# Performance work log

Hardware: AMD Instinct MI355X
Metric: run time of the kernel (lower is better)

## Reference

```python
import jax, jax.numpy as jnp
import numpy as np

D_MODEL = 1024
N_HEADS = 16


def setup_inputs() -> dict:
    key = jax.random.key(0)
    k1, k2, k3 = jax.random.split(key, 3)
    B, S = 2, 2048
    std_qkv = (2.0 / (D_MODEL + 3 * D_MODEL)) ** 0.5
    std_out = (2.0 / (D_MODEL + D_MODEL)) ** 0.5
    X = jax.random.normal(k1, (B, S, D_MODEL), dtype=jnp.float32)
    W_qkv = jax.random.normal(k2, (3 * D_MODEL, D_MODEL), dtype=jnp.float32) * std_qkv
    W_out = jax.random.normal(k3, (D_MODEL, D_MODEL), dtype=jnp.float32) * std_out
    return {"X": X, "W_qkv": W_qkv, "W_out": W_out}


def reference(X, W_qkv, W_out):
    B, S, D = X.shape
    H = N_HEADS
    dk = D // H
    # qkv projection: (..., d) @ W^T -> (..., 3d)
    qkv = jnp.einsum('bsd,ed->bse', X, W_qkv)
    Q, K, V = jnp.split(qkv, 3, axis=-1)
    # split heads: (B, S, H*dk) -> (B, H, S, dk)
    def heads(t):
        return t.reshape(B, S, H, dk).transpose(0, 2, 1, 3)
    Q, K, V = heads(Q), heads(K), heads(V)
    # scaled scores (B, H, S, S)
    scores = jnp.einsum('bhqd,bhkd->bhqk', Q, K) / jnp.sqrt(jnp.float32(dk))
    causal = jnp.tril(jnp.ones((S, S), dtype=bool))
    scores = jnp.where(causal, scores.astype(jnp.float32), -jnp.inf)
    weights = jax.nn.softmax(scores, axis=-1).astype(X.dtype)
    out = jnp.einsum('bhqk,bhkd->bhqd', weights, V)
    out = out.transpose(0, 2, 1, 3).reshape(B, S, D)
    return jnp.einsum('bsd,od->bso', out, W_out)
```

## Files before the change

### kernel.cpp

```cpp
#include <hip/hip_runtime.h>

typedef __bf16 bf16;
typedef __bf16 bf16x4v __attribute__((ext_vector_type(4)));
typedef __bf16 bf16x8 __attribute__((ext_vector_type(8)));
typedef float f32x4 __attribute__((ext_vector_type(4)));

#define MFMA16(a, b, c) __builtin_amdgcn_mfma_f32_16x16x32_bf16((a), (b), (c), 0, 0, 0)

#if __has_builtin(__builtin_amdgcn_exp2f)
#define EXP2(x) __builtin_amdgcn_exp2f(x)
#else
#define EXP2(x) exp2f(x)
#endif

#define SEQ 2048
#define DM 1024
#define NH 16

typedef __attribute__((address_space(3))) unsigned int lds_u32;
typedef __attribute__((address_space(1))) const unsigned int glb_u32;

__device__ __forceinline__ void gld16(const bf16* g, bf16* l) {
    __builtin_amdgcn_global_load_lds((glb_u32*)g, (lds_u32*)l, 16, 0, 0);
}

__global__ __launch_bounds__(256) void cvt_all(const float* __restrict__ X,
                                               const float* __restrict__ Wq,
                                               const float* __restrict__ Wo,
                                               bf16* __restrict__ Xb,
                                               bf16* __restrict__ Wqb,
                                               bf16* __restrict__ Wob) {
    const int i = blockIdx.x * 256 + threadIdx.x;
    const int N1 = (4 * 1024 * 1024) / 4;
    const int N2 = (3 * 1024 * 1024) / 4;
    const float* s; bf16* d; int off;
    if (i < N1)            { s = X;  d = Xb;  off = i; }
    else if (i < N1 + N2)  { s = Wq; d = Wqb; off = i - N1; }
    else                   { s = Wo; d = Wob; off = i - N1 - N2; }
    const float4 v = ((const float4*)s)[off];
    bf16x4v o;
    o.x = (bf16)v.x; o.y = (bf16)v.y; o.z = (bf16)v.z; o.w = (bf16)v.w;
    ((bf16x4v*)d)[off] = o;
}

__global__ __launch_bounds__(256) void gemm_qkv(const bf16* __restrict__ A,
                                                const bf16* __restrict__ B,
                                                bf16* __restrict__ qkbuf,
                                                bf16* __restrict__ vtg) {
    __shared__ bf16 smem[16384];
    bf16* As = smem;
    bf16* Bs = smem + 8192;

    const int K = DM, tid = threadIdx.x;
    const int lane = tid & 63, w = tid >> 6;
    const int quad = lane >> 4, l15 = lane & 15;
    const int wm = (w & 1) * 64, wn = (w >> 1) * 64;

    const int nbx = gridDim.x;
    const int orig = blockIdx.y * nbx + blockIdx.x;
    const int cpx = (nbx * gridDim.y) >> 3;
    const int swz = (orig & 7) * cpx + (orig >> 3);
    const int rowBase = (swz / nbx) * 128, colBase = (swz % nbx) * 128;
    const bool isV = (colBase >= 2 * DM);

    f32x4 acc[4][4] = {};

    auto stage = [&](int k0) {
#pragma unroll
        for (int i = 0; i < 4; ++i) {
            const int c = i * 256 + tid;
            const int row = c >> 3;
            const int sg = (c & 7) ^ (row & 7);
            gld16(A + (size_t)(rowBase + row) * K + k0 + sg * 8,
                  As + (i * 256 + w * 64) * 8);
            gld16(B + (size_t)(colBase + row) * K + k0 + sg * 8,
                  Bs + (i * 256 + w * 64) * 8);
        }
    };

    stage(0);

    for (int k0 = 0; k0 < K; k0 += 64) {
        __syncthreads();

        bf16x8 af[2][4], bfr[2][4];
#pragma unroll
        for (int ks = 0; ks < 2; ++ks)
#pragma unroll
            for (int i = 0; i < 4; ++i) {
                const int ra = wm + i * 16 + l15;
                af[ks][i]  = *(const bf16x8*)(As + ra * 64 + (((ks * 4 + quad) ^ (ra & 7)) * 8));
                const int rb = wn + i * 16 + l15;
                bfr[ks][i] = *(const bf16x8*)(Bs + rb * 64 + (((ks * 4 + quad) ^ (rb & 7)) * 8));
            }

        __syncthreads();

        if (k0 + 64 < K) stage(k0 + 64);

        if (isV) {
#pragma unroll
            for (int ks = 0; ks < 2; ++ks)
#pragma unroll
                for (int i = 0; i < 4; ++i)
#pragma unroll
                    for (int j = 0; j < 4; ++j)
                        acc[i][j] = MFMA16(af[ks][i], bfr[ks][j], acc[i][j]);
        } else {
#pragma unroll
            for (int ks = 0; ks < 2; ++ks)
#pragma unroll
                for (int i = 0; i < 4; ++i)
#pragma unroll
                    for (int j = 0; j < 4; ++j)
                        acc[i][j] = MFMA16(bfr[ks][j], af[ks][i], acc[i][j]);
        }
    }

    if (!isV) {
#pragma unroll
        for (int i = 0; i < 4; ++i)
#pragma unroll
            for (int j = 0; j < 4; ++j) {
                bf16x4v pk;
#pragma unroll
                for (int r = 0; r < 4; ++r) pk[r] = (bf16)acc[i][j][r];
                *(bf16x4v*)(qkbuf + (size_t)(rowBase + wm + i * 16 + l15) * 2048 +
                            colBase + wn + j * 16 + quad * 4) = pk;
            }
    } else {
        bf16* T = smem;
        const int vcolBase = colBase - 2 * DM;
        const int bb = rowBase >> 11;
        const int sBase = rowBase & 2047;
        const int drow0 = tid >> 4, seg = tid & 15;
#pragma unroll
        for (int c = 0; c < 2; ++c) {
            __syncthreads();
            if ((w >> 1) == c) {
#pragma unroll
                for (int i = 0; i < 4; ++i)
#pragma unroll
                    for (int j = 0; j < 4; ++j) {
                        bf16x4v pk;
#pragma unroll
                        for (int r = 0; r < 4; ++r) pk[r] = (bf16)acc[i][j][r];
                        *(bf16x4v*)(T + (j * 16 + l15) * 136 + wm + i * 16 + quad * 4) = pk;
                    }
            }
            __syncthreads();
#pragma unroll
            for (int rr = 0; rr < 4; ++rr) {
                const int drow = rr * 16 + drow0;
                *(bf16x8*)(vtg + (size_t)(bb * DM + vcolBase + c * 64 + drow) * SEQ +
                           sBase + seg * 8) =
                    *(const bf16x8*)(T + drow * 136 + seg * 8);
            }
        }
    }
}

__global__ __launch_bounds__(256) void gemm_out(const bf16* __restrict__ A,
                                                const bf16* __restrict__ B,
                                                float* __restrict__ C) {
    __shared__ bf16 As[64 * 64];
    __shared__ bf16 Bs[128 * 64];

    const int K = DM, N = DM, tid = threadIdx.x;
    const int lane = tid & 63, w = tid >> 6;
    const int quad = lane >> 4, l15 = lane & 15;
    const int wm = (w & 1) * 32, wn = (w >> 1) * 64;

    const int nbx = gridDim.x;
    const int orig = blockIdx.y * nbx + blockIdx.x;
    const int cpx = (nbx * gridDim.y) >> 3;
    const int swz = (orig & 7) * cpx + (orig >> 3);
    const int rowBase = (swz / nbx) * 64, colBase = (swz % nbx) * 128;

    f32x4 acc[2][4] = {};

    auto stage = [&](int k0) {
#pragma unroll
        for (int i = 0; i < 2; ++i) {
            const int c = i * 256 + tid;
            const int row = c >> 3;
            const int sg = (c & 7) ^ (row & 7);
            gld16(A + (size_t)(rowBase + row) * K + k0 + sg * 8,
                  As + (i * 256 + w * 64) * 8);
        }
#pragma unroll
        for (int i = 0; i < 4; ++i) {
            const int c = i * 256 + tid;
            const int row = c >> 3;
            const int sg = (c & 7) ^ (row & 7);
            gld16(B + (size_t)(colBase + row) * K + k0 + sg * 8,
                  Bs + (i * 256 + w * 64) * 8);
        }
    };

    stage(0);

    for (int k0 = 0; k0 < K; k0 += 64) {
        __syncthreads();

        bf16x8 af[2][2], bfr[2][4];
#pragma unroll
        for (int ks = 0; ks < 2; ++ks) {
#pragma unroll
            for (int i = 0; i < 2; ++i) {
                const int ra = wm + i * 16 + l15;
                af[ks][i] = *(const bf16x8*)(As + ra * 64 + (((ks * 4 + quad) ^ (ra & 7)) * 8));
            }
#pragma unroll
            for (int j = 0; j < 4; ++j) {
                const int rb = wn + j * 16 + l15;
                bfr[ks][j] = *(const bf16x8*)(Bs + rb * 64 + (((ks * 4 + quad) ^ (rb & 7)) * 8));
            }
        }

        __syncthreads();

        if (k0 + 64 < K) stage(k0 + 64);

#pragma unroll
        for (int ks = 0; ks < 2; ++ks)
#pragma unroll
            for (int i = 0; i < 2; ++i)
#pragma unroll
                for (int j = 0; j < 4; ++j)
                    acc[i][j] = MFMA16(bfr[ks][j], af[ks][i], acc[i][j]);
    }

#pragma unroll
    for (int i = 0; i < 2; ++i)
#pragma unroll
        for (int j = 0; j < 4; ++j)
            *(f32x4*)(C + (size_t)(rowBase + wm + i * 16 + l15) * N +
                      colBase + wn + j * 16 + quad * 4) = acc[i][j];
}

__global__ __launch_bounds__(128) void attn_fwd(const bf16* __restrict__ qk,
                                                const bf16* __restrict__ vtg,
                                                bf16* __restrict__ ao) {
    __shared__ bf16 Ks[64 * 64];
    __shared__ bf16 Vts[64 * 64];
    __shared__ bf16 Pb[2][2][16 * 72];

    const int tid = threadIdx.x;
    const int lane = tid & 63, w = tid >> 6;
    const int quad = lane >> 4, l15 = lane & 15;
    const int bh = blockIdx.x;
    const int b = bh >> 4, h = bh & 15;
    const int lo = blockIdx.y;
    const int hi = 63 - lo;
    const int g0 = lo * 32 + w * 16;
    const int g1 = hi * 32 + w * 16;

    const bf16* qkb   = qk + (size_t)b * SEQ * 2048;
    const bf16* kbase = qkb + DM + h * 64;
    const bf16* vb    = vtg + (size_t)bh * 64 * SEQ;

    auto stage = [&](int k0) {
#pragma unroll
        for (int i = 0; i < 4; ++i) {
            const int c = i * 128 + tid;
            const int row = c >> 3;
            const int sg = (c & 7) ^ (row & 7);
            gld16(kbase + (size_t)(k0 + row) * 2048 + sg * 8,
                  Ks + (i * 128 + w * 64) * 8);
            gld16(vb + (size_t)row * SEQ + k0 + sg * 8,
                  Vts + (i * 128 + w * 64) * 8);
        }
    };

    const int nkt = (hi + 2) >> 1;

    stage(0);

    const float SC = 0.125f * 1.44269504f;
    bf16x8 q0lo, q0hi, q1lo, q1hi;
    {
        const bf16* qp0 = qkb + (size_t)(g0 + l15) * 2048 + h * 64 + quad * 8;
        const bf16* qp1 = qkb + (size_t)(g1 + l15) * 2048 + h * 64 + quad * 8;
        bf16x8 a0 = *(const bf16x8*)qp0, c0 = *(const bf16x8*)(qp0 + 32);
        bf16x8 a1 = *(const bf16x8*)qp1, c1 = *(const bf16x8*)(qp1 + 32);
#pragma unroll
        for (int i = 0; i < 8; ++i) {
            q0lo[i] = (bf16)((float)a0[i] * SC);
            q0hi[i] = (bf16)((float)c0[i] * SC);
            q1lo[i] = (bf16)((float)a1[i] * SC);
            q1hi[i] = (bf16)((float)c1[i] * SC);
        }
    }

    bf16x8 onesf;
#pragma unroll
    for (int i = 0; i < 8; ++i) onesf[i] = (bf16)1.0f;

    f32x4 o0[4] = {}, o1[4] = {};
    f32x4 ol0 = {}, ol1 = {};

    for (int kt = 0; kt < nkt; ++kt) {
        const int k0 = kt * 64;
        __syncthreads();

        const bool live0 = (k0 <= g0 + 15);

        bf16x8 kf[8], vf[8];
#pragma unroll
        for (int t = 0; t < 4; ++t) {
            const int rk = t * 16 + l15;
            kf[2 * t]     = *(const bf16x8*)(Ks + rk * 64 + ((quad ^ (rk & 7)) * 8));
            kf[2 * t + 1] = *(const bf16x8*)(Ks + rk * 64 + (((4 + quad) ^ (rk & 7)) * 8));
            vf[2 * t]     = *(const bf16x8*)(Vts + rk * 64 + ((quad ^ (rk & 7)) * 8));
            vf[2 * t + 1] = *(const bf16x8*)(Vts + rk * 64 + (((4 + quad) ^ (rk & 7)) * 8));
        }

        __syncthreads();

        if (kt + 1 < nkt) stage(k0 + 64);

        f32x4 s0[4], s1[4];
#pragma unroll
        for (int t = 0; t < 4; ++t) {
            f32x4 z = {};
            z = MFMA16(kf[2 * t], q1lo, z);
            z = MFMA16(kf[2 * t + 1], q1hi, z);
            s1[t] = z;
            if (live0) {
                f32x4 y = {};
                y = MFMA16(kf[2 * t], q0lo, y);
                y = MFMA16(kf[2 * t + 1], q0hi, y);
                s0[t] = y;
            }
        }

        auto sfm = [&](f32x4* s, int g, bf16* P) {
            if (k0 + 63 > g) {
#pragma unroll
                for (int t = 0; t < 4; ++t)
#pragma unroll
                    for (int r = 0; r < 4; ++r)
                        if (k0 + t * 16 + quad * 4 + r > g + l15) s[t][r] = -1e30f;
            }
#pragma unroll
            for (int t = 0; t < 4; ++t) {
                bf16x4v pb4;
#pragma unroll
                for (int r = 0; r < 4; ++r) pb4[r] = (bf16)EXP2(s[t][r]);
                *(bf16x4v*)(P + l15 * 72 + t * 16 + quad * 4) = pb4;
            }
        };

        sfm(s1, g1, &Pb[w][1][0]);
        if (live0) sfm(s0, g0, &Pb[w][0][0]);

        asm volatile("s_waitcnt lgkmcnt(0)" ::: "memory");

        bf16x8 p1a = *(const bf16x8*)(&Pb[w][1][0] + l15 * 72 + quad * 8);
        bf16x8 p1b = *(const bf16x8*)(&Pb[w][1][0] + l15 * 72 + 32 + quad * 8);
        bf16x8 p0a, p0b;
        if (live0) {
            p0a = *(const bf16x8*)(&Pb[w][0][0] + l15 * 72 + quad * 8);
            p0b = *(const bf16x8*)(&Pb[w][0][0] + l15 * 72 + 32 + quad * 8);
        }

#pragma unroll
        for (int dt = 0; dt < 4; ++dt) {
            o1[dt] = MFMA16(vf[2 * dt], p1a, o1[dt]);
            o1[dt] = MFMA16(vf[2 * dt + 1], p1b, o1[dt]);
            if (live0) {
                o0[dt] = MFMA16(vf[2 * dt], p0a, o0[dt]);
                o0[dt] = MFMA16(vf[2 * dt + 1], p0b, o0[dt]);
            }
        }
        ol1 = MFMA16(onesf, p1a, ol1);
        ol1 = MFMA16(onesf, p1b, ol1);
        if (live0) {
            ol0 = MFMA16(onesf, p0a, ol0);
            ol0 = MFMA16(onesf, p0b, ol0);
        }
    }

    const float i0 = 1.f / ol0[0], i1 = 1.f / ol1[0];
    bf16* a0 = ao + (size_t)(b * SEQ + g0 + l15) * DM + h * 64;
    bf16* a1 = ao + (size_t)(b * SEQ + g1 + l15) * DM + h * 64;
#pragma unroll
    for (int dt = 0; dt < 4; ++dt) {
        bf16x4v v0, v1;
#pragma unroll
        for (int r = 0; r < 4; ++r) {
            v0[r] = (bf16)(o0[dt][r] * i0);
            v1[r] = (bf16)(o1[dt][r] * i1);
        }
        *(bf16x4v*)(a0 + dt * 16 + quad * 4) = v0;
        *(bf16x4v*)(a1 + dt * 16 + quad * 4) = v1;
    }
}

extern "C" void kernel_launch(void* const* d_in, const int* in_sizes, int n_in,
                              void* d_out, int out_size, void* d_ws, size_t ws_size,
                              hipStream_t stream) {
    const float* X    = (const float*)d_in[0];
    const float* Wqkv = (const float*)d_in[1];
    const float* Wout = (const float*)d_in[2];
    float* out = (float*)d_out;

    const int M = 2 * SEQ;
    const size_t nX    = (size_t)M * DM;
    const size_t nWqkv = (size_t)3 * DM * DM;
    const size_t nWout = (size_t)DM * DM;
    const size_t nQK   = (size_t)M * 2 * DM;
    const size_t nVT   = (size_t)2 * DM * SEQ;
    const size_t nAO   = (size_t)M * DM;

    if (ws_size < (nX + nWqkv + nWout + nQK + nVT + nAO) * sizeof(bf16)) return;

    bf16* Xb    = (bf16*)d_ws;
    bf16* Wqkvb = Xb + nX;
    bf16* Woutb = Wqkvb + nWqkv;
    bf16* qkbuf = Woutb + nWout;
    bf16* vtg   = qkbuf + nQK;
    bf16* ao    = vtg + nVT;

    const int nCvt4 = (int)((nX + nWqkv + nWout) / 4);
    cvt_all<<<dim3(nCvt4 / 256), 256, 0, stream>>>(X, Wqkv, Wout, Xb, Wqkvb, Woutb);

    gemm_qkv<<<dim3(3 * DM / 128, M / 128), 256, 0, stream>>>(Xb, Wqkvb, qkbuf, vtg);
    attn_fwd<<<dim3(2 * NH, SEQ / 64), 128, 0, stream>>>(qkbuf, vtg, ao);
    gemm_out<<<dim3(DM / 128, M / 64), 256, 0, stream>>>(ao, Woutb, out);
}
```

Before: 167.9 us.

## Drop paired causal query tiles in attention, launch one tile per block

The attention kernel previously paired a low and a high query tile in each block so every block did balanced causal work and shared each K/V tile load across both. Now each block handles a single 32-row query tile, with twice the grid size and heavy blocks scheduled first (reverse blockIdx.y order). This cuts per-block register and LDS use and allows more occupancy. In exchange each K/V tile is loaded once per query tile instead of being shared, and block lengths become uneven.

```diff
diff --git a/kernel.cpp b/kernel.cpp
--- a/kernel.cpp
+++ b/kernel.cpp
@@ -244,17 +244,15 @@
                                                 bf16* __restrict__ ao) {
     __shared__ bf16 Ks[64 * 64];
     __shared__ bf16 Vts[64 * 64];
-    __shared__ bf16 Pb[2][2][16 * 72];
+    __shared__ bf16 Pb[2][16 * 72];
 
     const int tid = threadIdx.x;
     const int lane = tid & 63, w = tid >> 6;
     const int quad = lane >> 4, l15 = lane & 15;
     const int bh = blockIdx.x;
     const int b = bh >> 4, h = bh & 15;
-    const int lo = blockIdx.y;
-    const int hi = 63 - lo;
-    const int g0 = lo * 32 + w * 16;
-    const int g1 = hi * 32 + w * 16;
+    const int qb = 63 - blockIdx.y;
+    const int g = qb * 32 + w * 16;
 
     const bf16* qkb   = qk + (size_t)b * SEQ * 2048;
     const bf16* kbase = qkb + DM + h * 64;
@@ -273,23 +271,19 @@
         }
     };
 
-    const int nkt = (hi + 2) >> 1;
+    const int nkt = ((qb * 32 + 31) >> 6) + 1;
 
     stage(0);
 
     const float SC = 0.125f * 1.44269504f;
-    bf16x8 q0lo, q0hi, q1lo, q1hi;
+    bf16x8 qlo, qhi;
     {
-        const bf16* qp0 = qkb + (size_t)(g0 + l15) * 2048 + h * 64 + quad * 8;
-        const bf16* qp1 = qkb + (size_t)(g1 + l15) * 2048 + h * 64 + quad * 8;
-        bf16x8 a0 = *(const bf16x8*)qp0, c0 = *(const bf16x8*)(qp0 + 32);
-        bf16x8 a1 = *(const bf16x8*)qp1, c1 = *(const bf16x8*)(qp1 + 32);
+        const bf16* qp = qkb + (size_t)(g + l15) * 2048 + h * 64 + quad * 8;
+        bf16x8 a = *(const bf16x8*)qp, c = *(const bf16x8*)(qp + 32);
 #pragma unroll
         for (int i = 0; i < 8; ++i) {
-            q0lo[i] = (bf16)((float)a0[i] * SC);
-            q0hi[i] = (bf16)((float)c0[i] * SC);
-            q1lo[i] = (bf16)((float)a1[i] * SC);
-            q1hi[i] = (bf16)((float)c1[i] * SC);
+            qlo[i] = (bf16)((float)a[i] * SC);
+            qhi[i] = (bf16)((float)c[i] * SC);
         }
     }
 
@@ -297,14 +291,12 @@
 #pragma unroll
     for (int i = 0; i < 8; ++i) onesf[i] = (bf16)1.0f;
 
-    f32x4 o0[4] = {}, o1[4] = {};
-    f32x4 ol0 = {}, ol1 = {};
+    f32x4 o[4] = {};
+    f32x4 ol = {};
 
     for (int kt = 0; kt < nkt; ++kt) {
         const int k0 = kt * 64;
         __syncthreads();
-
-        const bool live0 = (k0 <= g0 + 15);
 
         bf16x8 kf[8], vf[8];
 #pragma unroll
@@ -320,81 +312,53 @@
 
         if (kt + 1 < nkt) stage(k0 + 64);
 
-        f32x4 s0[4], s1[4];
+        f32x4 s[4];
 #pragma unroll
         for (int t = 0; t < 4; ++t) {
             f32x4 z = {};
-            z = MFMA16(kf[2 * t], q1lo, z);
-            z = MFMA16(kf[2 * t + 1], q1hi, z);
-            s1[t] = z;
-            if (live0) {
-                f32x4 y = {};
-                y = MFMA16(kf[2 * t], q0lo, y);
-                y = MFMA16(kf[2 * t + 1], q0hi, y);
-                s0[t] = y;
-            }
-        }
-
-        auto sfm = [&](f32x4* s, int g, bf16* P) {
-            if (k0 + 63 > g) {
-#pragma unroll
-                for (int t = 0; t < 4; ++t)
-#pragma unroll
-                    for (int r = 0; r < 4; ++r)
-                        if (k0 + t * 16 + quad * 4 + r > g + l15) s[t][r] = -1e30f;
-            }
-#pragma unroll
-            for (int t = 0; t < 4; ++t) {
-                bf16x4v pb4;
-#pragma unroll
-                for (int r = 0; r < 4; ++r) pb4[r] = (bf16)EXP2(s[t][r]);
-                *(bf16x4v*)(P + l15 * 72 + t * 16 + quad * 4) = pb4;
-            }
-        };
-
-        sfm(s1, g1, &Pb[w][1][0]);
-        if (live0) sfm(s0, g0, &Pb[w][0][0]);
+            z = MFMA16(kf[2 * t], qlo, z);
+            z = MFMA16(kf[2 * t + 1], qhi, z);
+            s[t] = z;
+        }
+
+        if (k0 + 63 > g) {
+#pragma unroll
+            for (int t = 0; t < 4; ++t)
+#pragma unroll
+                for (int r = 0; r < 4; ++r)
+                    if (k0 + t * 16 + quad * 4 + r > g + l15) s[t][r] = -1e30f;
+        }
+        bf16* P = &Pb[w][0];
+#pragma unroll
+        for (int t = 0; t < 4; ++t) {
+            bf16x4v pb4;
+#pragma unroll
+            for (int r = 0; r < 4; ++r) pb4[r] = (bf16)EXP2(s[t][r]);
+            *(bf16x4v*)(P + l15 * 72 + t * 16 + quad * 4) = pb4;
+        }
 
         asm volatile("s_waitcnt lgkmcnt(0)" ::: "memory");
 
-        bf16x8 p1a = *(const bf16x8*)(&Pb[w][1][0] + l15 * 72 + quad * 8);
-        bf16x8 p1b = *(const bf16x8*)(&Pb[w][1][0] + l15 * 72 + 32 + quad * 8);
-        bf16x8 p0a, p0b;
-        if (live0) {
-            p0a = *(const bf16x8*)(&Pb[w][0][0] + l15 * 72 + quad * 8);
-            p0b = *(const bf16x8*)(&Pb[w][0][0] + l15 * 72 + 32 + quad * 8);
-        }
+        bf16x8 pa = *(const bf16x8*)(P + l15 * 72 + quad * 8);
+        bf16x8 pb = *(const bf16x8*)(P + l15 * 72 + 32 + quad * 8);
 
 #pragma unroll
         for (int dt = 0; dt < 4; ++dt) {
-            o1[dt] = MFMA16(vf[2 * dt], p1a, o1[dt]);
-            o1[dt] = MFMA16(vf[2 * dt + 1], p1b, o1[dt]);
-            if (live0) {
-                o0[dt] = MFMA16(vf[2 * dt], p0a, o0[dt]);
-                o0[dt] = MFMA16(vf[2 * dt + 1], p0b, o0[dt]);
-            }
-        }
-        ol1 = MFMA16(onesf, p1a, ol1);
-        ol1 = MFMA16(onesf, p1b, ol1);
-        if (live0) {
-            ol0 = MFMA16(onesf, p0a, ol0);
-            ol0 = MFMA16(onesf, p0b, ol0);
-        }
-    }
-
-    const float i0 = 1.f / ol0[0], i1 = 1.f / ol1[0];
-    bf16* a0 = ao + (size_t)(b * SEQ + g0 + l15) * DM + h * 64;
-    bf16* a1 = ao + (size_t)(b * SEQ + g1 + l15) * DM + h * 64;
+            o[dt] = MFMA16(vf[2 * dt], pa, o[dt]);
+            o[dt] = MFMA16(vf[2 * dt + 1], pb, o[dt]);
+        }
+        ol = MFMA16(onesf, pa, ol);
+        ol = MFMA16(onesf, pb, ol);
+    }
+
+    const float inv = 1.f / ol[0];
+    bf16* a = ao + (size_t)(b * SEQ + g + l15) * DM + h * 64;
 #pragma unroll
     for (int dt = 0; dt < 4; ++dt) {
-        bf16x4v v0, v1;
-#pragma unroll
-        for (int r = 0; r < 4; ++r) {
-            v0[r] = (bf16)(o0[dt][r] * i0);
-            v1[r] = (bf16)(o1[dt][r] * i1);
-        }
-        *(bf16x4v*)(a0 + dt * 16 + quad * 4) = v0;
-        *(bf16x4v*)(a1 + dt * 16 + quad * 4) = v1;
+        bf16x4v v;
+#pragma unroll
+        for (int r = 0; r < 4; ++r) v[r] = (bf16)(o[dt][r] * inv);
+        *(bf16x4v*)(a + dt * 16 + quad * 4) = v;
     }
 }
 
@@ -427,6 +391,6 @@
     cvt_all<<<dim3(nCvt4 / 256), 256, 0, stream>>>(X, Wqkv, Wout, Xb, Wqkvb, Woutb);
 
     gemm_qkv<<<dim3(3 * DM / 128, M / 128), 256, 0, stream>>>(Xb, Wqkvb, qkbuf, vtg);
-    attn_fwd<<<dim3(2 * NH, SEQ / 64), 128, 0, stream>>>(qkbuf, vtg, ao);
+    attn_fwd<<<dim3(2 * NH, SEQ / 32), 128, 0, stream>>>(qkbuf, vtg, ao);
     gemm_out<<<dim3(DM / 128, M / 64), 256, 0, stream>>>(ao, Woutb, out);
 }
```

After: 171.5 us. 2.1% more time.
